# Performance work log

Measured on AMD Instinct MI355X. Metric: run time of the kernel, lower is better.

Reference implementation:

```python
import jax, jax.numpy as jnp
import numpy as np

N_IN = 500000
N_OUT = 125000
K = 8          # kernel^dim = 2^3 offsets
R = 62500      # rulebook pairs per offset (strided conv: total == N_IN)
RS = 62500     # submanifold rulebook pairs per offset
C_IN = 64
C_OUT = 128
BN_EPS = 1e-4  # scn.BatchNormReLU default eps


def bn_relu(x, gamma, beta):
    # SCN BatchNormReLU in training mode: per-channel stats over active sites.
    m = jnp.mean(x, axis=0)
    v = jnp.var(x, axis=0)
    return jax.nn.relu((x - m) * jax.lax.rsqrt(v + BN_EPS) * gamma + beta)


def sparse_conv(x, W, in_idx, out_idx, n_out):
    # rulebook gather-GEMM-scatter.
    # x: [N_in, Cin]; W: [K, Cin, Cout]; in_idx/out_idx: [K, R]
    g = x[in_idx]                                   # [K, R, Cin] gather
    c = jnp.einsum('krc,kcd->krd', g, W)            # per-offset GEMM
    out = jnp.zeros((n_out, W.shape[-1]), x.dtype)
    return out.at[out_idx.reshape(-1)].add(c.reshape(-1, W.shape[-1]))


def setup_inputs() -> dict:
    key = jax.random.key(0)
    ks = jax.random.split(key, 8)
    x = jax.random.normal(ks[0], (N_IN, C_IN), dtype=jnp.float32)
    W1 = jax.random.normal(ks[1], (K, C_IN, C_OUT), dtype=jnp.float32) / np.sqrt(K * C_IN)
    Ws = jax.random.normal(ks[2], (K, C_OUT, C_OUT), dtype=jnp.float32) / np.sqrt(K * C_OUT)
    W2 = jax.random.normal(ks[3], (K, C_IN, C_OUT), dtype=jnp.float32) / np.sqrt(K * C_IN)
    in_idx1 = jax.random.randint(ks[4], (K, R), 0, N_IN, dtype=jnp.int32)
    out_idx1 = jax.random.randint(ks[5], (K, R), 0, N_OUT, dtype=jnp.int32)
    in_idx_s = jax.random.randint(ks[6], (K, RS), 0, N_OUT, dtype=jnp.int32)
    out_idx_s = jax.random.randint(ks[7], (K, RS), 0, N_OUT, dtype=jnp.int32)
    return {
        'x': x,
        'gamma1': jnp.ones((C_IN,), jnp.float32),
        'beta1': jnp.zeros((C_IN,), jnp.float32),
        'gamma2': jnp.ones((C_OUT,), jnp.float32),
        'beta2': jnp.zeros((C_OUT,), jnp.float32),
        'W1': W1, 'Ws': Ws, 'W2': W2,
        'in_idx1': in_idx1, 'out_idx1': out_idx1,
        'in_idx_s': in_idx_s, 'out_idx_s': out_idx_s,
        'n_out': N_OUT,
    }


def reference(x, gamma1, beta1, gamma2, beta2, W1, Ws, W2,
              in_idx1, out_idx1, in_idx_s, out_idx_s, n_out):
    x1 = bn_relu(x, gamma1, beta1)                              # bnr1
    y1 = sparse_conv(x1, W1, in_idx1, out_idx1, n_out)          # conv1 (stride 2)
    y1 = bn_relu(y1, gamma2, beta2)                             # bnr2
    y1 = sparse_conv(y1, Ws, in_idx_s, out_idx_s, n_out)        # submanifold conv
    y2 = sparse_conv(x1, W2, in_idx1, out_idx1, n_out)          # conv2 (same rulebook)
    return y1 + y2                                              # AddTable
```

## Files before the change

### kernel.cpp

```cpp
#include <hip/hip_runtime.h>

#define K_OFF   8
#define R_PAIRS 62500
#define NPAIRS  500000
#define N_IN    500000
#define N_OUT   125000
#define CIN     64
#define COUT    128
#define BN_EPS  1e-4f
#define SCAN_ELEMS 4096
#define NBINS_KC (N_OUT * K_OFF)
#define NSB_KC  245
#define BM      32
#define CHUNK   64
#define OLD_TILES 8

typedef __bf16 bf16;
typedef __bf16 bf16x4 __attribute__((ext_vector_type(4)));
typedef __bf16 bf16x8 __attribute__((ext_vector_type(8)));
typedef float  f32x4  __attribute__((ext_vector_type(4)));
typedef unsigned int u32;

__device__ __forceinline__ int zb(int row, int col_bf16) {
    int byte = (row << 10) + (col_bf16 << 1);
    return byte ^ ((row & 7) << 4);
}

template<int C>
__global__ void bn_stats_kernel(const float* __restrict__ x, int n_rows,
                                float* __restrict__ sums ) {
    constexpr int CG = C / 4;
    int tid = blockIdx.x * blockDim.x + threadIdx.x;
    int nth = gridDim.x * blockDim.x;
    const float4* x4 = (const float4*)x;
    long n4 = (long)n_rows * CG;
    int cg = tid % CG;
    float s[4] = {0,0,0,0}, q[4] = {0,0,0,0};
    for (long i = tid; i < n4; i += nth) {
        float4 v = x4[i];
        float f[4] = {v.x, v.y, v.z, v.w};
        #pragma unroll
        for (int j = 0; j < 4; j++) { s[j] += f[j]; q[j] += f[j] * f[j]; }
    }
    __shared__ float acc[2 * C];
    for (int i = threadIdx.x; i < 2 * C; i += blockDim.x) acc[i] = 0.f;
    __syncthreads();
    #pragma unroll
    for (int j = 0; j < 4; j++) {
        atomicAdd(&acc[cg * 4 + j], s[j]);
        atomicAdd(&acc[C + cg * 4 + j], q[j]);
    }
    __syncthreads();
    for (int i = threadIdx.x; i < 2 * C; i += blockDim.x) atomicAdd(&sums[i], acc[i]);
}

template<int C>
__global__ void bn_finalize_kernel(const float* __restrict__ sums,
                                   const float* __restrict__ gamma,
                                   const float* __restrict__ beta,
                                   float inv_n, float* __restrict__ ss) {
    int c = threadIdx.x;
    if (c < C) {
        float m  = sums[c] * inv_n;
        float v  = sums[C + c] * inv_n - m * m;
        float sc = gamma[c] * rsqrtf(v + BN_EPS);
        ss[c]     = sc;
        ss[C + c] = beta[c] - m * sc;
    }
}

__global__ void bn_finalize2_kernel(const float* __restrict__ S ,
                                    const float* __restrict__ gamma,
                                    const float* __restrict__ beta,
                                    float* __restrict__ ss) {
    int c = threadIdx.x;
    float s = 0.f, q = 0.f;
    for (int st = 0; st < 64; st++) { s += S[st * 256 + c]; q += S[st * 256 + 128 + c]; }
    float m = s / (float)N_OUT;
    float v = q / (float)N_OUT - m * m;
    float sc = gamma[c] * rsqrtf(v + BN_EPS);
    ss[c] = sc; ss[128 + c] = beta[c] - m * sc;
}

__global__ void pack12_kernel(const float* __restrict__ W1, const float* __restrict__ W2,
                              bf16* __restrict__ Wf) {
    int idx = blockIdx.x * 256 + threadIdx.x;
    int j = idx & 7;
    int lane = (idx >> 3) & 63;
    int fi = idx >> 9;
    int ks = fi >> 4, nfrag = fi & 15;
    int k512 = ks * 32 + (lane >> 4) * 8 + j;
    int koff = k512 >> 6, kc = k512 & 63;
    int c = nfrag * 16 + (lane & 15);
    const float* W = (c < 128) ? W1 : W2;
    Wf[idx] = (bf16)W[((long)koff * CIN + kc) * COUT + (c & 127)];
}

__global__ void packS_kernel(const float* __restrict__ Ws, bf16* __restrict__ Wf) {
    int idx = blockIdx.x * 256 + threadIdx.x;
    int j = idx & 7;
    int lane = (idx >> 3) & 63;
    int fi = idx >> 9;
    int ksg = fi >> 3, nfrag = fi & 7;
    int k1024 = ksg * 32 + (lane >> 4) * 8 + j;
    int koff = k1024 >> 7, kc = k1024 & 127;
    int c = nfrag * 16 + (lane & 15);
    Wf[idx] = (bf16)Ws[((long)koff * COUT + kc) * COUT + c];
}

__global__ void histOK_kernel(const int* __restrict__ oidx, u32* __restrict__ counts) {
    int p = blockIdx.x * blockDim.x + threadIdx.x;
    int stride = gridDim.x * blockDim.x;
    for (; p < NPAIRS; p += stride) {
        int bin = oidx[p] * K_OFF + p / R_PAIRS;
        atomicAdd(&counts[bin], 1u);
    }
}

__global__ void scan1_kernel(const u32* __restrict__ counts, u32* __restrict__ bsum, int n) {
    __shared__ u32 sd[256];
    int tid = threadIdx.x;
    int base = blockIdx.x * SCAN_ELEMS + tid * 16;
    u32 s = 0;
    #pragma unroll
    for (int j = 0; j < 16; j++) { int i = base + j; if (i < n) s += counts[i]; }
    sd[tid] = s; __syncthreads();
    for (int st = 128; st > 0; st >>= 1) { if (tid < st) sd[tid] += sd[tid + st]; __syncthreads(); }
    if (tid == 0) bsum[blockIdx.x] = sd[0];
}

__global__ void scan2_kernel(u32* __restrict__ bsum, u32* __restrict__ starts, int nb, int n) {
    __shared__ u32 sd[256];
    int tid = threadIdx.x;
    u32 v = (tid < nb) ? bsum[tid] : 0;
    sd[tid] = v; __syncthreads();
    for (int st = 1; st < 256; st <<= 1) {
        u32 t = (tid >= st) ? sd[tid - st] : 0;
        __syncthreads();
        sd[tid] += t;
        __syncthreads();
    }
    if (tid < nb) bsum[tid] = sd[tid] - v;
    if (tid == 255) starts[n] = sd[255];
}

__global__ void scan3_kernel(const u32* __restrict__ counts, const u32* __restrict__ bsum,
                             u32* __restrict__ starts, int n) {
    __shared__ u32 sd[256];
    int tid = threadIdx.x;
    int base = blockIdx.x * SCAN_ELEMS + tid * 16;
    u32 v[16]; u32 s = 0;
    #pragma unroll
    for (int j = 0; j < 16; j++) { int i = base + j; v[j] = (i < n) ? counts[i] : 0; s += v[j]; }
    sd[tid] = s; __syncthreads();
    for (int st = 1; st < 256; st <<= 1) {
        u32 t = (tid >= st) ? sd[tid - st] : 0;
        __syncthreads();
        sd[tid] += t;
        __syncthreads();
    }
    u32 run = bsum[blockIdx.x] + sd[tid] - s;
    #pragma unroll
    for (int j = 0; j < 16; j++) { int i = base + j; if (i < n) starts[i] = run; run += v[j]; }
}

__global__ void buildF_kernel(const int* __restrict__ iidx, const int* __restrict__ oidx,
                              const u32* __restrict__ kstart, u32* __restrict__ counts,
                              u32* __restrict__ listF) {
    int p = blockIdx.x * 256 + threadIdx.x;
    if (p >= NPAIRS) return;
    int bin = oidx[p] * K_OFF + p / R_PAIRS;
    u32 c = atomicSub(&counts[bin], 1u);
    listF[kstart[bin] + c - 1u] = (u32)iidx[p];
}

__global__ __launch_bounds__(512) void fused12_kernel(
    const float* __restrict__ x, const bf16* __restrict__ Wf, const float* __restrict__ ss1,
    const u32* __restrict__ kstart, const u32* __restrict__ listF,
    bf16* __restrict__ y1, bf16* __restrict__ y2b, float* __restrict__ sums2s)
{
    __shared__ bf16 z[BM * 512];
    __shared__ bf16 As[CHUNK * 64];
    __shared__ float s_sc[64], s_sh[64];
    int tid = threadIdx.x, lane = tid & 63, wave = tid >> 6;
    int o0 = blockIdx.x * BM;
    int nrow = min(BM, N_OUT - o0);
    if (tid < 64) { s_sc[tid] = ss1[tid]; s_sh[tid] = ss1[64 + tid]; }

    int row = tid >> 4, sl = tid & 15;
    int ch0 = (sl & 1) * 32;
    u32 sA = 0, eA = 0;
    if (row < nrow) {
        size_t bin = (size_t)(o0 + row) * K_OFF + (sl >> 1);
        sA = kstart[bin]; eA = kstart[bin + 1];
    }
    u32 lo  = kstart[(size_t)o0 * K_OFF];
    u32 hiS = kstart[(size_t)(o0 + nrow) * K_OFF];

    f32x4 a[8];
    #pragma unroll
    for (int g = 0; g < 8; g++) a[g] = (f32x4)(0.f);

    for (u32 cb = lo; cb < hiS; cb += CHUNK) {
        u32 cEnd = min(cb + (u32)CHUNK, hiS);
        int nE = (int)(cEnd - cb);
        __syncthreads();
        #pragma unroll
        for (int r = 0; r < 2; r++) {
            int slot = r * 32 + (tid >> 4);
            if (slot < nE) {
                u32 in = listF[cb + slot];
                int cpos = (tid & 15) * 4;
                float4 v = *(const float4*)(x + (size_t)in * 64 + cpos);
                float f[4] = {v.x, v.y, v.z, v.w};
                bf16x4 h;
                #pragma unroll
                for (int j = 0; j < 4; j++)
                    h[j] = (bf16)fmaxf(f[j] * s_sc[cpos + j] + s_sh[cpos + j], 0.f);
                *(bf16x4*)((char*)As + ((slot * 128 + cpos * 2) ^ ((slot & 7) << 4))) = h;
            }
        }
        __syncthreads();
        u32 pa = max(sA, cb), pb = min(eA, cEnd);
        for (u32 p = pa; p < pb; p++) {
            int slot = (int)(p - cb);
            #pragma unroll
            for (int u = 0; u < 4; u++) {
                int bo = (slot * 128 + ch0 * 2 + u * 16) ^ ((slot & 7) << 4);
                int4 vi = *(const int4*)((const char*)As + bo);
                bf16x8 hv = *(bf16x8*)&vi;
                #pragma unroll
                for (int j = 0; j < 8; j++)
                    a[u * 2 + (j >> 2)][j & 3] += (float)hv[j];
            }
        }
    }
    __syncthreads();

    {
        int colb = sl * 32;
        #pragma unroll
        for (int u = 0; u < 4; u++) {
            bf16x8 h;
            #pragma unroll
            for (int j = 0; j < 8; j++) h[j] = (bf16)a[u * 2 + (j >> 2)][j & 3];
            *(bf16x8*)((char*)z + zb(row, colb + u * 8)) = h;
        }
    }
    __syncthreads();

    int l15 = lane & 15, kr0 = (lane >> 4) * 8;
    f32x4 acc[2][2];
    #pragma unroll
    for (int m = 0; m < 2; m++)
        #pragma unroll
        for (int nf = 0; nf < 2; nf++) acc[m][nf] = (f32x4)(0.f);

    for (int ks = 0; ks < 16; ks++) {
        int colb = ks * 32 + kr0;
        bf16x8 af0 = *(bf16x8*)((char*)z + zb(l15, colb));
        bf16x8 af1 = *(bf16x8*)((char*)z + zb(l15 + 16, colb));
        #pragma unroll
        for (int nf = 0; nf < 2; nf++) {
            bf16x8 bf = *(const bf16x8*)(Wf + ((size_t)(ks * 16 + wave * 2 + nf) * 64 + lane) * 8);
            acc[0][nf] = __builtin_amdgcn_mfma_f32_16x16x32_bf16(af0, bf, acc[0][nf], 0, 0, 0);
            acc[1][nf] = __builtin_amdgcn_mfma_f32_16x16x32_bf16(af1, bf, acc[1][nf], 0, 0, 0);
        }
    }
    __syncthreads();

    bf16* st = z;
    int rb = (lane >> 4) * 4;
    #pragma unroll
    for (int m = 0; m < 2; m++)
        #pragma unroll
        for (int nf = 0; nf < 2; nf++)
            #pragma unroll
            for (int j = 0; j < 4; j++)
                st[(m * 16 + rb + j) * 256 + wave * 32 + nf * 16 + l15] = (bf16)acc[m][nf][j];
    __syncthreads();

    if (tid < 128) {
        float s = 0.f, q = 0.f;
        for (int r = 0; r < nrow; r++) { float v = (float)st[r * 256 + tid]; s += v; q += v * v; }
        int sb = (blockIdx.x & 63) * 256;
        atomicAdd(&sums2s[sb + tid], s);
        atomicAdd(&sums2s[sb + 128 + tid], q);
    }
    {
        int orow = tid >> 4, seg = tid & 15;
        if (orow < nrow) {
            const int4* src = (const int4*)(st + orow * 256 + seg * 16);
            int4 v0 = src[0], v1 = src[1];
            bf16* dst = (seg < 8) ? (y1  + (size_t)(o0 + orow) * 128 + seg * 16)
                                  : (y2b + (size_t)(o0 + orow) * 128 + (seg - 8) * 16);
            ((int4*)dst)[0] = v0; ((int4*)dst)[1] = v1;
        }
    }
}

__global__ __launch_bounds__(512) void fusedS_kernel(
    const bf16* __restrict__ y1, const bf16* __restrict__ Wf, const float* __restrict__ ss2,
    const u32* __restrict__ kstart, const u32* __restrict__ listF,
    const bf16* __restrict__ y2b, float* __restrict__ out)
{
    __shared__ bf16 z[BM * 512];
    __shared__ bf16 As[CHUNK * 128];
    __shared__ float s_sc[128], s_sh[128];
    int tid = threadIdx.x, lane = tid & 63, wave = tid >> 6;
    int o0 = blockIdx.x * BM;
    int nrow = min(BM, N_OUT - o0);
    if (tid < 128) { s_sc[tid] = ss2[tid]; s_sh[tid] = ss2[128 + tid]; }

    int row = tid >> 4, sl = tid & 15;
    int kq = sl >> 2, ch0 = (sl & 3) * 32;
    u32 sA = 0, eA = 0, sB = 0, eB = 0;
    if (row < nrow) {
        size_t binb = (size_t)(o0 + row) * K_OFF;
        sA = kstart[binb + kq];     eA = kstart[binb + kq + 1];
        sB = kstart[binb + 4 + kq]; eB = kstart[binb + 4 + kq + 1];
    }
    u32 lo  = kstart[(size_t)o0 * K_OFF];
    u32 hiS = kstart[(size_t)(o0 + nrow) * K_OFF];

    f32x4 aA[8], aB[8];
    #pragma unroll
    for (int g = 0; g < 8; g++) { aA[g] = (f32x4)(0.f); aB[g] = (f32x4)(0.f); }

    for (u32 cb = lo; cb < hiS; cb += CHUNK) {
        u32 cEnd = min(cb + (u32)CHUNK, hiS);
        int nE = (int)(cEnd - cb);
        __syncthreads();
        #pragma unroll
        for (int r = 0; r < 2; r++) {
            int slot = r * 32 + (tid >> 4);
            if (slot < nE) {
                u32 in = listF[cb + slot];
                int cpos = (tid & 15) * 8;
                int4 vi = *(const int4*)(y1 + (size_t)in * 128 + cpos);
                bf16x8 hv = *(bf16x8*)&vi;
                bf16x8 ho;
                #pragma unroll
                for (int j = 0; j < 8; j++)
                    ho[j] = (bf16)fmaxf((float)hv[j] * s_sc[cpos + j] + s_sh[cpos + j], 0.f);
                *(bf16x8*)((char*)As + ((slot * 256 + cpos * 2) ^ ((slot & 7) << 4))) = ho;
            }
        }
        __syncthreads();
        u32 pa = max(sA, cb), pb = min(eA, cEnd);
        for (u32 p = pa; p < pb; p++) {
            int slot = (int)(p - cb);
            #pragma unroll
            for (int u = 0; u < 4; u++) {
                int bo = (slot * 256 + ch0 * 2 + u * 16) ^ ((slot & 7) << 4);
                int4 vi = *(const int4*)((const char*)As + bo);
                bf16x8 hv = *(bf16x8*)&vi;
                #pragma unroll
                for (int j = 0; j < 8; j++)
                    aA[u * 2 + (j >> 2)][j & 3] += (float)hv[j];
            }
        }
        pa = max(sB, cb); pb = min(eB, cEnd);
        for (u32 p = pa; p < pb; p++) {
            int slot = (int)(p - cb);
            #pragma unroll
            for (int u = 0; u < 4; u++) {
                int bo = (slot * 256 + ch0 * 2 + u * 16) ^ ((slot & 7) << 4);
                int4 vi = *(const int4*)((const char*)As + bo);
                bf16x8 hv = *(bf16x8*)&vi;
                #pragma unroll
                for (int j = 0; j < 8; j++)
                    aB[u * 2 + (j >> 2)][j & 3] += (float)hv[j];
            }
        }
    }

    int l15 = lane & 15, kr0 = (lane >> 4) * 8;
    f32x4 acc[2];
    acc[0] = (f32x4)(0.f); acc[1] = (f32x4)(0.f);
    int colb0 = sl * 32;

    #pragma unroll
    for (int h = 0; h < 2; h++) {
        __syncthreads();
        {
            #pragma unroll
            for (int u = 0; u < 4; u++) {
                bf16x8 hv;
                #pragma unroll
                for (int j = 0; j < 8; j++)
                    hv[j] = (bf16)((h == 0 ? aA : aB)[u * 2 + (j >> 2)][j & 3]);
                *(bf16x8*)((char*)z + zb(row, colb0 + u * 8)) = hv;
            }
        }
        __syncthreads();

        for (int ks = 0; ks < 16; ks++) {
            int colb = ks * 32 + kr0;
            bf16x8 af0 = *(bf16x8*)((char*)z + zb(l15, colb));
            bf16x8 af1 = *(bf16x8*)((char*)z + zb(l15 + 16, colb));
            int fi = (h * 16 + ks) * 8 + wave;
            bf16x8 bf = *(const bf16x8*)(Wf + ((size_t)fi * 64 + lane) * 8);
            acc[0] = __builtin_amdgcn_mfma_f32_16x16x32_bf16(af0, bf, acc[0], 0, 0, 0);
            acc[1] = __builtin_amdgcn_mfma_f32_16x16x32_bf16(af1, bf, acc[1], 0, 0, 0);
        }
    }
    __syncthreads();

    float* zf = (float*)z;
    int rb = (lane >> 4) * 4;
    #pragma unroll
    for (int m = 0; m < 2; m++)
        #pragma unroll
        for (int j = 0; j < 4; j++)
            zf[(m * 16 + rb + j) * 128 + wave * 16 + l15] = acc[m][j];
    __syncthreads();

    {
        int orow = tid >> 4, seg = tid & 15;
        if (orow < nrow) {
            f32x4 s0 = *(f32x4*)&zf[orow * 128 + seg * 8];
            f32x4 s1 = *(f32x4*)&zf[orow * 128 + seg * 8 + 4];
            int4 yv = *(const int4*)(y2b + (size_t)(o0 + orow) * 128 + seg * 8);
            bf16x8 hy = *(bf16x8*)&yv;
            float4 w0 = make_float4(s0[0] + (float)hy[0], s0[1] + (float)hy[1],
                                    s0[2] + (float)hy[2], s0[3] + (float)hy[3]);
            float4 w1 = make_float4(s1[0] + (float)hy[4], s1[1] + (float)hy[5],
                                    s1[2] + (float)hy[6], s1[3] + (float)hy[7]);
            float* dst = out + (size_t)(o0 + orow) * 128 + seg * 8;
            *(float4*)dst = w0;
            *(float4*)(dst + 4) = w1;
        }
    }
}

__global__ __launch_bounds__(256) void conv12_atomic_kernel(
    const float* __restrict__ x,
    const float* __restrict__ W1, const float* __restrict__ W2,
    const int* __restrict__ in_idx, const int* __restrict__ out_idx,
    const float* __restrict__ ss1,
    float* __restrict__ y1, float* __restrict__ y2)
{
    int k    = blockIdx.y;
    int tid  = threadIdx.x;
    int wave = tid >> 6, lane = tid & 63;

    __shared__ bf16 As[64 * 64];
    __shared__ int  s_out[64];
    __shared__ float s_sc[64], s_sh[64];
    char* asb = (char*)As;

    if (tid < 64) { s_sc[tid] = ss1[tid]; s_sh[tid] = ss1[64 + tid]; }

    const float* Wk = ((wave & 2) ? W2 : W1) + (long)k * CIN * COUT;
    int nbase = (wave & 1) * 64;
    int l15 = lane & 15;
    int kr0 = (lane >> 4) * 8;

    bf16x8 bfrag[2][4];
    #pragma unroll
    for (int ks = 0; ks < 2; ks++)
        #pragma unroll
        for (int nf = 0; nf < 4; nf++) {
            const float* p = Wk + (long)(ks * 32 + kr0) * COUT + nbase + nf * 16 + l15;
            bf16x8 b;
            #pragma unroll
            for (int j = 0; j < 8; j++) b[j] = (bf16)p[(long)j * COUT];
            bfrag[ks][nf] = b;
        }

    const int* in_k  = in_idx  + k * R_PAIRS;
    const int* out_k = out_idx + k * R_PAIRS;
    float* ybase = (wave & 2) ? y2 : y1;

    int grow = tid >> 2;
    int gcol = (tid & 3) * 16;

    __syncthreads();

    for (int t = 0; t < OLD_TILES; t++) {
        int pair0 = blockIdx.x * (OLD_TILES * 64) + t * 64;
        {
            int p = pair0 + grow;
            bool valid = p < R_PAIRS;
            long src = valid ? (long)in_k[p] : 0;
            const float4* xr = (const float4*)(x + src * CIN + gcol);
            #pragma unroll
            for (int g = 0; g < 2; g++) {
                float4 va = make_float4(0, 0, 0, 0), vb = va;
                if (valid) { va = xr[g * 2]; vb = xr[g * 2 + 1]; }
                float f[8] = {va.x, va.y, va.z, va.w, vb.x, vb.y, vb.z, vb.w};
                bf16x8 h;
                #pragma unroll
                for (int j = 0; j < 8; j++) {
                    int c = gcol + g * 8 + j;
                    h[j] = (bf16)fmaxf(f[j] * s_sc[c] + s_sh[c], 0.f);
                }
                int boff = ((grow * 128) + (gcol + g * 8) * 2) ^ ((grow & 7) << 4);
                *(bf16x8*)(asb + boff) = h;
            }
        }
        if (tid < 64) {
            int p = pair0 + tid;
            s_out[tid] = (p < R_PAIRS) ? out_k[p] : -1;
        }
        __syncthreads();

        f32x4 acc[4][4];
        #pragma unroll
        for (int m = 0; m < 4; m++)
            #pragma unroll
            for (int n = 0; n < 4; n++) acc[m][n] = (f32x4)(0.f);

        #pragma unroll
        for (int ks = 0; ks < 2; ks++) {
            bf16x8 af[4];
            #pragma unroll
            for (int m = 0; m < 4; m++) {
                int rrow = m * 16 + l15;
                int boff = (rrow * 128 + (ks * 32 + kr0) * 2) ^ ((rrow & 7) << 4);
                af[m] = *(bf16x8*)(asb + boff);
            }
            #pragma unroll
            for (int m = 0; m < 4; m++)
                #pragma unroll
                for (int nf = 0; nf < 4; nf++)
                    acc[m][nf] = __builtin_amdgcn_mfma_f32_16x16x32_bf16(
                        af[m], bfrag[ks][nf], acc[m][nf], 0, 0, 0);
        }

        int rbase = (lane >> 4) * 4;
        #pragma unroll
        for (int m = 0; m < 4; m++)
            #pragma unroll
            for (int j = 0; j < 4; j++) {
                int o = s_out[m * 16 + rbase + j];
                if (o >= 0)
                    #pragma unroll
                    for (int nf = 0; nf < 4; nf++)
                        atomicAdd(&ybase[(long)o * COUT + nbase + nf * 16 + l15],
                                  acc[m][nf][j]);
            }
        __syncthreads();
    }
}

__global__ __launch_bounds__(256) void convs_atomic_kernel(
    const float* __restrict__ y1,
    const float* __restrict__ Ws,
    const int* __restrict__ in_idx, const int* __restrict__ out_idx,
    const float* __restrict__ ss2,
    float* __restrict__ out)
{
    int k    = blockIdx.y;
    int tid  = threadIdx.x;
    int wave = tid >> 6, lane = tid & 63;

    __shared__ bf16 As[64 * 128];
    __shared__ int  s_out[64];
    __shared__ float s_sc[128], s_sh[128];
    char* asb = (char*)As;

    if (tid < 128) { s_sc[tid] = ss2[tid]; s_sh[tid] = ss2[128 + tid]; }

    const float* Wk = Ws + (long)k * COUT * COUT;
    int nbase = wave * 32;
    int l15 = lane & 15;
    int kr0 = (lane >> 4) * 8;

    bf16x8 bfrag[4][2];
    #pragma unroll
    for (int ks = 0; ks < 4; ks++)
        #pragma unroll
        for (int nf = 0; nf < 2; nf++) {
            const float* p = Wk + (long)(ks * 32 + kr0) * COUT + nbase + nf * 16 + l15;
            bf16x8 b;
            #pragma unroll
            for (int j = 0; j < 8; j++) b[j] = (bf16)p[(long)j * COUT];
            bfrag[ks][nf] = b;
        }

    const int* in_k  = in_idx  + k * R_PAIRS;
    const int* out_k = out_idx + k * R_PAIRS;

    int grow = tid >> 2;
    int gcol = (tid & 3) * 32;

    __syncthreads();

    for (int t = 0; t < OLD_TILES; t++) {
        int pair0 = blockIdx.x * (OLD_TILES * 64) + t * 64;
        {
            int p = pair0 + grow;
            bool valid = p < R_PAIRS;
            long src = valid ? (long)in_k[p] : 0;
            const float4* yr = (const float4*)(y1 + src * COUT + gcol);
            #pragma unroll
            for (int g = 0; g < 4; g++) {
                float4 va = make_float4(0, 0, 0, 0), vb = va;
                if (valid) { va = yr[g * 2]; vb = yr[g * 2 + 1]; }
                float f[8] = {va.x, va.y, va.z, va.w, vb.x, vb.y, vb.z, vb.w};
                bf16x8 h;
                #pragma unroll
                for (int j = 0; j < 8; j++) {
                    int c = gcol + g * 8 + j;
                    h[j] = (bf16)fmaxf(f[j] * s_sc[c] + s_sh[c], 0.f);
                }
                int boff = (grow * 256 + (gcol + g * 8) * 2) ^ ((grow & 7) << 4);
                *(bf16x8*)(asb + boff) = h;
            }
        }
        if (tid < 64) {
            int p = pair0 + tid;
            s_out[tid] = (p < R_PAIRS) ? out_k[p] : -1;
        }
        __syncthreads();

        f32x4 acc[4][2];
        #pragma unroll
        for (int m = 0; m < 4; m++)
            #pragma unroll
            for (int n = 0; n < 2; n++) acc[m][n] = (f32x4)(0.f);

        #pragma unroll
        for (int ks = 0; ks < 4; ks++) {
            bf16x8 af[4];
            #pragma unroll
            for (int m = 0; m < 4; m++) {
                int rrow = m * 16 + l15;
                int boff = (rrow * 256 + (ks * 32 + kr0) * 2) ^ ((rrow & 7) << 4);
                af[m] = *(bf16x8*)(asb + boff);
            }
            #pragma unroll
            for (int m = 0; m < 4; m++)
                #pragma unroll
                for (int nf = 0; nf < 2; nf++)
                    acc[m][nf] = __builtin_amdgcn_mfma_f32_16x16x32_bf16(
                        af[m], bfrag[ks][nf], acc[m][nf], 0, 0, 0);
        }

        int rbase = (lane >> 4) * 4;
        #pragma unroll
        for (int m = 0; m < 4; m++)
            #pragma unroll
            for (int j = 0; j < 4; j++) {
                int o = s_out[m * 16 + rbase + j];
                if (o >= 0)
                    #pragma unroll
                    for (int nf = 0; nf < 2; nf++)
                        atomicAdd(&out[(long)o * COUT + nbase + nf * 16 + l15],
                                  acc[m][nf][j]);
            }
        __syncthreads();
    }
}

extern "C" void kernel_launch(void* const* d_in, const int* in_sizes, int n_in,
                              void* d_out, int out_size, void* d_ws, size_t ws_size,
                              hipStream_t stream) {
    const float* x       = (const float*)d_in[0];
    const float* gamma1  = (const float*)d_in[1];
    const float* beta1   = (const float*)d_in[2];
    const float* gamma2  = (const float*)d_in[3];
    const float* beta2   = (const float*)d_in[4];
    const float* W1      = (const float*)d_in[5];
    const float* Ws      = (const float*)d_in[6];
    const float* W2      = (const float*)d_in[7];
    const int*   in_idx1   = (const int*)d_in[8];
    const int*   out_idx1  = (const int*)d_in[9];
    const int*   in_idx_s  = (const int*)d_in[10];
    const int*   out_idx_s = (const int*)d_in[11];

    float* out = (float*)d_out;
    char*  ws  = (char*)d_ws;

    auto a256 = [](size_t v) { return (v + 255) & ~(size_t)255; };

    size_t off_y1      = 0;
    size_t off_y2b     = a256(off_y1 + 32000000);
    size_t off_stats   = a256(off_y2b + 32000000);
    size_t off_s2s     = a256(off_stats + 4096);
    size_t off_countsA = a256(off_s2s + 65536);
    size_t off_countsB = off_countsA + 4ull * NBINS_KC;
    size_t off_kstartA = a256(off_countsB + 4ull * NBINS_KC);
    size_t off_kstartB = a256(off_kstartA + 4ull * (NBINS_KC + 1));
    size_t off_bsum    = a256(off_kstartB + 4ull * (NBINS_KC + 1));
    size_t off_listA   = a256(off_bsum + 1024);
    size_t off_listB   = a256(off_listA + 4 * NPAIRS);
    size_t off_wf12    = a256(off_listB + 4 * NPAIRS);
    size_t off_wfs     = a256(off_wf12 + 262144);
    size_t need        = off_wfs + 262144;

    if (need > ws_size) {
        float* y1f   = (float*)ws;
        float* stats = y1f + (long)N_OUT * COUT;
        float* sums1 = stats;
        float* ss1   = stats + 128;
        float* sums2 = stats + 256;
        float* ss2   = stats + 512;

        hipMemsetAsync(d_out, 0, (size_t)N_OUT * COUT * 4, stream);
        hipMemsetAsync(d_ws,  0, (size_t)N_OUT * COUT * 4 + 768 * 4, stream);

        bn_stats_kernel<64><<<1024, 256, 0, stream>>>(x, N_IN, sums1);
        bn_finalize_kernel<64><<<1, 64, 0, stream>>>(sums1, gamma1, beta1, 1.f / N_IN, ss1);

        dim3 cgrid((R_PAIRS + OLD_TILES * 64 - 1) / (OLD_TILES * 64), K_OFF);
        conv12_atomic_kernel<<<cgrid, 256, 0, stream>>>(x, W1, W2, in_idx1, out_idx1, ss1, y1f, out);

        bn_stats_kernel<128><<<1024, 256, 0, stream>>>(y1f, N_OUT, sums2);
        bn_finalize_kernel<128><<<1, 128, 0, stream>>>(sums2, gamma2, beta2, 1.f / N_OUT, ss2);

        convs_atomic_kernel<<<cgrid, 256, 0, stream>>>(y1f, Ws, in_idx_s, out_idx_s, ss2, out);
        return;
    }

    bf16*  y1      = (bf16*)(ws + off_y1);
    bf16*  y2b     = (bf16*)(ws + off_y2b);
    float* sums1   = (float*)(ws + off_stats);
    float* ss1     = sums1 + 256;
    float* ss2     = sums1 + 512;
    float* s2s     = (float*)(ws + off_s2s);
    u32*   countsA = (u32*)(ws + off_countsA);
    u32*   countsB = (u32*)(ws + off_countsB);
    u32*   kstartA = (u32*)(ws + off_kstartA);
    u32*   kstartB = (u32*)(ws + off_kstartB);
    u32*   bsum    = (u32*)(ws + off_bsum);
    u32*   listA   = (u32*)(ws + off_listA);
    u32*   listB   = (u32*)(ws + off_listB);
    bf16*  wf12    = (bf16*)(ws + off_wf12);
    bf16*  wfs     = (bf16*)(ws + off_wfs);

    int nblk = (N_OUT + BM - 1) / BM;

    hipMemsetAsync(ws + off_stats, 0, off_countsA - off_stats, stream);
    hipMemsetAsync(countsA, 0, 8ull * NBINS_KC, stream);

    histOK_kernel<<<512, 256, 0, stream>>>(out_idx1, countsA);
    histOK_kernel<<<512, 256, 0, stream>>>(out_idx_s, countsB);
    scan1_kernel<<<NSB_KC, 256, 0, stream>>>(countsA, bsum, NBINS_KC);
    scan2_kernel<<<1, 256, 0, stream>>>(bsum, kstartA, NSB_KC, NBINS_KC);
    scan3_kernel<<<NSB_KC, 256, 0, stream>>>(countsA, bsum, kstartA, NBINS_KC);
    scan1_kernel<<<NSB_KC, 256, 0, stream>>>(countsB, bsum, NBINS_KC);
    scan2_kernel<<<1, 256, 0, stream>>>(bsum, kstartB, NSB_KC, NBINS_KC);
    scan3_kernel<<<NSB_KC, 256, 0, stream>>>(countsB, bsum, kstartB, NBINS_KC);
    buildF_kernel<<<(NPAIRS + 255) / 256, 256, 0, stream>>>(in_idx1, out_idx1, kstartA, countsA, listA);
    buildF_kernel<<<(NPAIRS + 255) / 256, 256, 0, stream>>>(in_idx_s, out_idx_s, kstartB, countsB, listB);

    bn_stats_kernel<64><<<1024, 256, 0, stream>>>(x, N_IN, sums1);
    bn_finalize_kernel<64><<<1, 64, 0, stream>>>(sums1, gamma1, beta1, 1.f / N_IN, ss1);
    pack12_kernel<<<512, 256, 0, stream>>>(W1, W2, wf12);
    packS_kernel<<<512, 256, 0, stream>>>(Ws, wfs);

    fused12_kernel<<<nblk, 512, 0, stream>>>(x, wf12, ss1, kstartA, listA, y1, y2b, s2s);
    bn_finalize2_kernel<<<1, 128, 0, stream>>>(s2s, gamma2, beta2, ss2);

    fusedS_kernel<<<nblk, 512, 0, stream>>>(y1, wfs, ss2, kstartB, listB, y2b, out);
}
```

Before: 392.7 us.

## Merge rulebook build passes and register-prefetch next gather chunk

Combines the two histogram, scan and list-build passes into single launches over a concatenated bin space, which roughly halves the preprocessing kernel launches. The two fused conv kernels now use 32-row chunks and issue the global gather for the next chunk into registers before accumulating the current one, so load latency overlaps with LDS accumulation. The trade-off is twice as many chunk iterations and barriers in exchange for a single in-flight gather per thread. The second conv relies on the combined kstart offsets pointing into the merged list.

```diff
diff --git a/kernel.cpp b/kernel.cpp
--- a/kernel.cpp
+++ b/kernel.cpp
@@ -8,11 +8,12 @@
 #define CIN     64
 #define COUT    128
 #define BN_EPS  1e-4f
-#define SCAN_ELEMS 4096
 #define NBINS_KC (N_OUT * K_OFF)
-#define NSB_KC  245
+#define NB2     (2 * NBINS_KC)
+#define SCAN_E2 8192
+#define NSB2    245
 #define BM      32
-#define CHUNK   64
+#define CHUNK   32
 #define OLD_TILES 8
 
 typedef __bf16 bf16;
@@ -108,11 +109,14 @@
     Wf[idx] = (bf16)Ws[((long)koff * COUT + kc) * COUT + c];
 }
 
-__global__ void histOK_kernel(const int* __restrict__ oidx, u32* __restrict__ counts) {
+__global__ void hist2_kernel(const int* __restrict__ o1, const int* __restrict__ os,
+                             u32* __restrict__ counts) {
     int p = blockIdx.x * blockDim.x + threadIdx.x;
     int stride = gridDim.x * blockDim.x;
-    for (; p < NPAIRS; p += stride) {
-        int bin = oidx[p] * K_OFF + p / R_PAIRS;
+    for (; p < 2 * NPAIRS; p += stride) {
+        int bin;
+        if (p < NPAIRS) bin = o1[p] * K_OFF + p / R_PAIRS;
+        else { int q = p - NPAIRS; bin = NBINS_KC + os[q] * K_OFF + q / R_PAIRS; }
         atomicAdd(&counts[bin], 1u);
     }
 }
@@ -120,10 +124,10 @@
 __global__ void scan1_kernel(const u32* __restrict__ counts, u32* __restrict__ bsum, int n) {
     __shared__ u32 sd[256];
     int tid = threadIdx.x;
-    int base = blockIdx.x * SCAN_ELEMS + tid * 16;
+    int base = blockIdx.x * SCAN_E2 + tid * 32;
     u32 s = 0;
     #pragma unroll
-    for (int j = 0; j < 16; j++) { int i = base + j; if (i < n) s += counts[i]; }
+    for (int j = 0; j < 32; j++) { int i = base + j; if (i < n) s += counts[i]; }
     sd[tid] = s; __syncthreads();
     for (int st = 128; st > 0; st >>= 1) { if (tid < st) sd[tid] += sd[tid + st]; __syncthreads(); }
     if (tid == 0) bsum[blockIdx.x] = sd[0];
@@ -148,10 +152,10 @@
                              u32* __restrict__ starts, int n) {
     __shared__ u32 sd[256];
     int tid = threadIdx.x;
-    int base = blockIdx.x * SCAN_ELEMS + tid * 16;
-    u32 v[16]; u32 s = 0;
-    #pragma unroll
-    for (int j = 0; j < 16; j++) { int i = base + j; v[j] = (i < n) ? counts[i] : 0; s += v[j]; }
+    int base = blockIdx.x * SCAN_E2 + tid * 32;
+    u32 v[32]; u32 s = 0;
+    #pragma unroll
+    for (int j = 0; j < 32; j++) { int i = base + j; v[j] = (i < n) ? counts[i] : 0; s += v[j]; }
     sd[tid] = s; __syncthreads();
     for (int st = 1; st < 256; st <<= 1) {
         u32 t = (tid >= st) ? sd[tid - st] : 0;
@@ -161,17 +165,20 @@
     }
     u32 run = bsum[blockIdx.x] + sd[tid] - s;
     #pragma unroll
-    for (int j = 0; j < 16; j++) { int i = base + j; if (i < n) starts[i] = run; run += v[j]; }
-}
-
-__global__ void buildF_kernel(const int* __restrict__ iidx, const int* __restrict__ oidx,
-                              const u32* __restrict__ kstart, u32* __restrict__ counts,
-                              u32* __restrict__ listF) {
+    for (int j = 0; j < 32; j++) { int i = base + j; if (i < n) starts[i] = run; run += v[j]; }
+}
+
+__global__ void buildF2_kernel(const int* __restrict__ i1, const int* __restrict__ o1,
+                               const int* __restrict__ is, const int* __restrict__ os,
+                               const u32* __restrict__ kstart, u32* __restrict__ counts,
+                               u32* __restrict__ listF) {
     int p = blockIdx.x * 256 + threadIdx.x;
-    if (p >= NPAIRS) return;
-    int bin = oidx[p] * K_OFF + p / R_PAIRS;
+    if (p >= 2 * NPAIRS) return;
+    int bin, in;
+    if (p < NPAIRS) { bin = o1[p] * K_OFF + p / R_PAIRS; in = i1[p]; }
+    else { int q = p - NPAIRS; bin = NBINS_KC + os[q] * K_OFF + q / R_PAIRS; in = is[q]; }
     u32 c = atomicSub(&counts[bin], 1u);
-    listF[kstart[bin] + c - 1u] = (u32)iidx[p];
+    listF[kstart[bin] + c - 1u] = (u32)in;
 }
 
 __global__ __launch_bounds__(512) void fused12_kernel(
@@ -197,31 +204,35 @@
     u32 lo  = kstart[(size_t)o0 * K_OFF];
     u32 hiS = kstart[(size_t)(o0 + nrow) * K_OFF];
 
+    int esl  = tid >> 4;
+    int cpos = (tid & 15) * 4;
+    float4 pv;
+
+    auto issue = [&](u32 base) {
+        u32 idx = base + esl;
+        u32 in = (idx < hiS) ? listF[idx] : 0u;
+        pv = *(const float4*)(x + (size_t)in * 64 + cpos);
+    };
+
     f32x4 a[8];
     #pragma unroll
     for (int g = 0; g < 8; g++) a[g] = (f32x4)(0.f);
 
+    if (lo < hiS) issue(lo);
     for (u32 cb = lo; cb < hiS; cb += CHUNK) {
-        u32 cEnd = min(cb + (u32)CHUNK, hiS);
-        int nE = (int)(cEnd - cb);
-        __syncthreads();
-        #pragma unroll
-        for (int r = 0; r < 2; r++) {
-            int slot = r * 32 + (tid >> 4);
-            if (slot < nE) {
-                u32 in = listF[cb + slot];
-                int cpos = (tid & 15) * 4;
-                float4 v = *(const float4*)(x + (size_t)in * 64 + cpos);
-                float f[4] = {v.x, v.y, v.z, v.w};
-                bf16x4 h;
-                #pragma unroll
-                for (int j = 0; j < 4; j++)
-                    h[j] = (bf16)fmaxf(f[j] * s_sc[cpos + j] + s_sh[cpos + j], 0.f);
-                *(bf16x4*)((char*)As + ((slot * 128 + cpos * 2) ^ ((slot & 7) << 4))) = h;
-            }
-        }
-        __syncthreads();
-        u32 pa = max(sA, cb), pb = min(eA, cEnd);
+        int nE = (int)min((u32)CHUNK, hiS - cb);
+        __syncthreads();
+        if (esl < nE) {
+            float f[4] = {pv.x, pv.y, pv.z, pv.w};
+            bf16x4 h;
+            #pragma unroll
+            for (int j = 0; j < 4; j++)
+                h[j] = (bf16)fmaxf(f[j] * s_sc[cpos + j] + s_sh[cpos + j], 0.f);
+            *(bf16x4*)((char*)As + ((esl * 128 + cpos * 2) ^ ((esl & 7) << 4))) = h;
+        }
+        __syncthreads();
+        if (cb + CHUNK < hiS) issue(cb + CHUNK);
+        u32 pa = max(sA, cb), pb = min(eA, cb + (u32)CHUNK);
         for (u32 p = pa; p < pb; p++) {
             int slot = (int)(p - cb);
             #pragma unroll
@@ -323,31 +334,35 @@
     u32 lo  = kstart[(size_t)o0 * K_OFF];
     u32 hiS = kstart[(size_t)(o0 + nrow) * K_OFF];
 
+    int esl  = tid >> 4;
+    int cpos = (tid & 15) * 8;
+    int4 pv;
+
+    auto issue = [&](u32 base) {
+        u32 idx = base + esl;
+        u32 in = (idx < hiS) ? listF[idx] : 0u;
+        pv = *(const int4*)(y1 + (size_t)in * 128 + cpos);
+    };
+
     f32x4 aA[8], aB[8];
     #pragma unroll
     for (int g = 0; g < 8; g++) { aA[g] = (f32x4)(0.f); aB[g] = (f32x4)(0.f); }
 
+    if (lo < hiS) issue(lo);
     for (u32 cb = lo; cb < hiS; cb += CHUNK) {
-        u32 cEnd = min(cb + (u32)CHUNK, hiS);
-        int nE = (int)(cEnd - cb);
-        __syncthreads();
-        #pragma unroll
-        for (int r = 0; r < 2; r++) {
-            int slot = r * 32 + (tid >> 4);
-            if (slot < nE) {
-                u32 in = listF[cb + slot];
-                int cpos = (tid & 15) * 8;
-                int4 vi = *(const int4*)(y1 + (size_t)in * 128 + cpos);
-                bf16x8 hv = *(bf16x8*)&vi;
-                bf16x8 ho;
-                #pragma unroll
-                for (int j = 0; j < 8; j++)
-                    ho[j] = (bf16)fmaxf((float)hv[j] * s_sc[cpos + j] + s_sh[cpos + j], 0.f);
-                *(bf16x8*)((char*)As + ((slot * 256 + cpos * 2) ^ ((slot & 7) << 4))) = ho;
-            }
-        }
-        __syncthreads();
-        u32 pa = max(sA, cb), pb = min(eA, cEnd);
+        int nE = (int)min((u32)CHUNK, hiS - cb);
+        __syncthreads();
+        if (esl < nE) {
+            bf16x8 hv = *(bf16x8*)&pv;
+            bf16x8 ho;
+            #pragma unroll
+            for (int j = 0; j < 8; j++)
+                ho[j] = (bf16)fmaxf((float)hv[j] * s_sc[cpos + j] + s_sh[cpos + j], 0.f);
+            *(bf16x8*)((char*)As + ((esl * 256 + cpos * 2) ^ ((esl & 7) << 4))) = ho;
+        }
+        __syncthreads();
+        if (cb + CHUNK < hiS) issue(cb + CHUNK);
+        u32 pa = max(sA, cb), pb = min(eA, cb + (u32)CHUNK);
         for (u32 p = pa; p < pb; p++) {
             int slot = (int)(p - cb);
             #pragma unroll
@@ -360,7 +375,7 @@
                     aA[u * 2 + (j >> 2)][j & 3] += (float)hv[j];
             }
         }
-        pa = max(sB, cb); pb = min(eB, cEnd);
+        pa = max(sB, cb); pb = min(eB, cb + (u32)CHUNK);
         for (u32 p = pa; p < pb; p++) {
             int slot = (int)(p - cb);
             #pragma unroll
@@ -680,14 +695,11 @@
     size_t off_y2b     = a256(off_y1 + 32000000);
     size_t off_stats   = a256(off_y2b + 32000000);
     size_t off_s2s     = a256(off_stats + 4096);
-    size_t off_countsA = a256(off_s2s + 65536);
-    size_t off_countsB = off_countsA + 4ull * NBINS_KC;
-    size_t off_kstartA = a256(off_countsB + 4ull * NBINS_KC);
-    size_t off_kstartB = a256(off_kstartA + 4ull * (NBINS_KC + 1));
-    size_t off_bsum    = a256(off_kstartB + 4ull * (NBINS_KC + 1));
-    size_t off_listA   = a256(off_bsum + 1024);
-    size_t off_listB   = a256(off_listA + 4 * NPAIRS);
-    size_t off_wf12    = a256(off_listB + 4 * NPAIRS);
+    size_t off_counts  = a256(off_s2s + 65536);
+    size_t off_kstart  = a256(off_counts + 4ull * NB2);
+    size_t off_bsum    = a256(off_kstart + 4ull * (NB2 + 1));
+    size_t off_list    = a256(off_bsum + 1024);
+    size_t off_wf12    = a256(off_list + 4ull * 2 * NPAIRS);
     size_t off_wfs     = a256(off_wf12 + 262144);
     size_t need        = off_wfs + 262144;
 
@@ -721,39 +733,32 @@
     float* ss1     = sums1 + 256;
     float* ss2     = sums1 + 512;
     float* s2s     = (float*)(ws + off_s2s);
-    u32*   countsA = (u32*)(ws + off_countsA);
-    u32*   countsB = (u32*)(ws + off_countsB);
-    u32*   kstartA = (u32*)(ws + off_kstartA);
-    u32*   kstartB = (u32*)(ws + off_kstartB);
+    u32*   counts  = (u32*)(ws + off_counts);
+    u32*   kstart  = (u32*)(ws + off_kstart);
     u32*   bsum    = (u32*)(ws + off_bsum);
-    u32*   listA   = (u32*)(ws + off_listA);
-    u32*   listB   = (u32*)(ws + off_listB);
+    u32*   list    = (u32*)(ws + off_list);
     bf16*  wf12    = (bf16*)(ws + off_wf12);
     bf16*  wfs     = (bf16*)(ws + off_wfs);
 
     int nblk = (N_OUT + BM - 1) / BM;
 
-    hipMemsetAsync(ws + off_stats, 0, off_countsA - off_stats, stream);
-    hipMemsetAsync(countsA, 0, 8ull * NBINS_KC, stream);
-
-    histOK_kernel<<<512, 256, 0, stream>>>(out_idx1, countsA);
-    histOK_kernel<<<512, 256, 0, stream>>>(out_idx_s, countsB);
-    scan1_kernel<<<NSB_KC, 256, 0, stream>>>(countsA, bsum, NBINS_KC);
-    scan2_kernel<<<1, 256, 0, stream>>>(bsum, kstartA, NSB_KC, NBINS_KC);
-    scan3_kernel<<<NSB_KC, 256, 0, stream>>>(countsA, bsum, kstartA, NBINS_KC);
-    scan1_kernel<<<NSB_KC, 256, 0, stream>>>(countsB, bsum, NBINS_KC);
-    scan2_kernel<<<1, 256, 0, stream>>>(bsum, kstartB, NSB_KC, NBINS_KC);
-    scan3_kernel<<<NSB_KC, 256, 0, stream>>>(countsB, bsum, kstartB, NBINS_KC);
-    buildF_kernel<<<(NPAIRS + 255) / 256, 256, 0, stream>>>(in_idx1, out_idx1, kstartA, countsA, listA);
-    buildF_kernel<<<(NPAIRS + 255) / 256, 256, 0, stream>>>(in_idx_s, out_idx_s, kstartB, countsB, listB);
+    hipMemsetAsync(ws + off_stats, 0, off_counts - off_stats, stream);
+    hipMemsetAsync(counts, 0, 4ull * NB2, stream);
+
+    hist2_kernel<<<1024, 256, 0, stream>>>(out_idx1, out_idx_s, counts);
+    scan1_kernel<<<NSB2, 256, 0, stream>>>(counts, bsum, NB2);
+    scan2_kernel<<<1, 256, 0, stream>>>(bsum, kstart, NSB2, NB2);
+    scan3_kernel<<<NSB2, 256, 0, stream>>>(counts, bsum, kstart, NB2);
+    buildF2_kernel<<<(2 * NPAIRS + 255) / 256, 256, 0, stream>>>(
+        in_idx1, out_idx1, in_idx_s, out_idx_s, kstart, counts, list);
 
     bn_stats_kernel<64><<<1024, 256, 0, stream>>>(x, N_IN, sums1);
     bn_finalize_kernel<64><<<1, 64, 0, stream>>>(sums1, gamma1, beta1, 1.f / N_IN, ss1);
     pack12_kernel<<<512, 256, 0, stream>>>(W1, W2, wf12);
     packS_kernel<<<512, 256, 0, stream>>>(Ws, wfs);
 
-    fused12_kernel<<<nblk, 512, 0, stream>>>(x, wf12, ss1, kstartA, listA, y1, y2b, s2s);
+    fused12_kernel<<<nblk, 512, 0, stream>>>(x, wf12, ss1, kstart, list, y1, y2b, s2s);
     bn_finalize2_kernel<<<1, 128, 0, stream>>>(s2s, gamma2, beta2, ss2);
 
-    fusedS_kernel<<<nblk, 512, 0, stream>>>(y1, wfs, ss2, kstartB, listB, y2b, out);
-}
+    fusedS_kernel<<<nblk, 512, 0, stream>>>(y1, wfs, ss2, kstart + NBINS_KC, list, y2b, out);
+}
```

After: 384.3 us. 2.1% less time.
